# Kernel optimization log

Hardware: AMD Instinct MI355X
Metric: run time of the kernel (lower is better)

Reference implementation:

```python
import jax, jax.numpy as jnp
import numpy as np

N, IN, HID, OUT = 8192, 512, 256, 128

def setup_inputs() -> dict:
    key = jax.random.key(0)
    k1, k2, k3, k4 = jax.random.split(key, 4)
    adj = jax.random.uniform(k1, (N, N), dtype=jnp.float32)
    feature = jax.random.normal(k2, (N, IN), dtype=jnp.float32)
    W1 = jax.random.normal(k3, (IN, HID), dtype=jnp.float32) * (1.0 / np.sqrt(IN))
    b1 = jnp.zeros((HID,), dtype=jnp.float32)
    W2 = jax.random.normal(k4, (HID, OUT), dtype=jnp.float32) * (1.0 / np.sqrt(HID))
    b2 = jnp.zeros((OUT,), dtype=jnp.float32)
    return {"adj": adj, "feature": feature, "W1": W1, "b1": b1, "W2": W2, "b2": b2}

def reference(adj, feature, W1, b1, W2, b2):
    # GCN encoder: layer1 (relu) then layer2 (linear output)
    h = jax.nn.relu(adj @ (feature @ W1) + b1)   # [N, HID]
    h = adj @ (h @ W2) + b2                      # [N, OUT]
    # InnerProductDecoder: sigmoid(flatten(h @ h.T))
    logits = h @ h.T                             # [N, N]
    h_noise = jax.nn.sigmoid(logits.reshape(-1)) # [N*N]
    return (h_noise, h)
```

## Files before the change

kernel.cpp:

```cpp
#include <hip/hip_runtime.h>


typedef __bf16 bf16x8_t __attribute__((ext_vector_type(8)));
typedef __bf16 bf16x4_t __attribute__((ext_vector_type(4)));
typedef float  f32x4_t  __attribute__((ext_vector_type(4)));

#define MFMA_BF16(a, b, c) __builtin_amdgcn_mfma_f32_16x16x32_bf16((a), (b), (c), 0, 0, 0)

__device__ __forceinline__ bf16x8_t cvt8(f32x4_t u, f32x4_t v) {
    bf16x8_t o;
    o[0] = (__bf16)u[0]; o[1] = (__bf16)u[1]; o[2] = (__bf16)u[2]; o[3] = (__bf16)u[3];
    o[4] = (__bf16)v[0]; o[5] = (__bf16)v[1]; o[6] = (__bf16)v[2]; o[7] = (__bf16)v[3];
    return o;
}

__device__ __forceinline__ f32x4_t nt_load4(const float* p) {
    return __builtin_nontemporal_load((const f32x4_t*)p);
}
__device__ __forceinline__ void nt_store4(f32x4_t v, float* p) {
    __builtin_nontemporal_store(v, (f32x4_t*)p);
}

template<int AUX>
__device__ __forceinline__ void gload_lds16(const float* g, float* l) {
    __builtin_amdgcn_global_load_lds(
        (const __attribute__((address_space(1))) unsigned int*)g,
        (__attribute__((address_space(3))) unsigned int*)l, 16, 0, AUX);
}

__global__ __launch_bounds__(256) void cast_all(
    const float* __restrict__ feat, const float* __restrict__ W1,
    const float* __restrict__ W2, __bf16* __restrict__ fb,
    __bf16* __restrict__ w1t, __bf16* __restrict__ w2t)
{
    const int j = blockIdx.x * 256 + threadIdx.x;
    if (j < 524288) {
        const float* p = feat + (size_t)j * 8;
        f32x4_t u = nt_load4(p);
        f32x4_t v = nt_load4(p + 4);
        *(bf16x8_t*)(fb + (size_t)j * 8) = cvt8(u, v);
    } else if (j < 524288 + 131072) {
        int t = j - 524288;
        int k = t >> 8, n = t & 255;
        w1t[n * 512 + k] = (__bf16)W1[t];
    } else if (j < 524288 + 131072 + 32768) {
        int t = j - 655360;
        int k = t >> 7, n = t & 127;
        w2t[n * 256 + k] = (__bf16)W2[t];
    }
}

template<int MT, int WC>
__global__ __launch_bounds__(256, 2) void gemm_bt_cbf16(
    const __bf16* __restrict__ X, const __bf16* __restrict__ Yb,
    __bf16* __restrict__ C, int K, int N)
{
    constexpr int WR = 4 / WC;
    constexpr int BM = WR * MT * 16;
    constexpr int BN = WC * 64;
    const int mblk = blockIdx.x, nblk = blockIdx.y;
    const int w = threadIdx.x >> 6, lane = threadIdx.x & 63;
    const int wr = w / WC, wc = w % WC;
    const int q = lane >> 4, l16 = lane & 15;
    const int mbase = mblk * BM + wr * (MT * 16);
    const int nbase = nblk * BN + wc * 64;

    f32x4_t acc[MT][4];
    const f32x4_t z = {0.f, 0.f, 0.f, 0.f};
#pragma unroll
    for (int i = 0; i < MT; i++)
#pragma unroll
        for (int jj = 0; jj < 4; jj++) acc[i][jj] = z;

    const __bf16* Xr[MT];
    const __bf16* Yr[4];
#pragma unroll
    for (int i = 0; i < MT; i++) Xr[i] = X + (size_t)(mbase + i * 16 + l16) * K + q * 8;
#pragma unroll
    for (int jj = 0; jj < 4; jj++) Yr[jj] = Yb + (size_t)(nbase + jj * 16 + l16) * K + q * 8;

    for (int k = 0; k < K; k += 32) {
        bf16x8_t a[MT], b[4];
#pragma unroll
        for (int i = 0; i < MT; i++) a[i] = *(const bf16x8_t*)(Xr[i] + k);
#pragma unroll
        for (int jj = 0; jj < 4; jj++) b[jj] = *(const bf16x8_t*)(Yr[jj] + k);
#pragma unroll
        for (int i = 0; i < MT; i++)
#pragma unroll
            for (int jj = 0; jj < 4; jj++) acc[i][jj] = MFMA_BF16(a[i], b[jj], acc[i][jj]);
    }

#pragma unroll
    for (int i = 0; i < MT; i++)
#pragma unroll
        for (int jj = 0; jj < 4; jj++) {
            const int row0 = mbase + i * 16 + q * 4;
            const int col = nbase + jj * 16 + l16;
#pragma unroll
            for (int r = 0; r < 4; r++)
                C[(size_t)(row0 + r) * N + col] = (__bf16)acc[i][jj][r];
        }
}

template<int NN>
__global__ __launch_bounds__(256, 2) void gemm_adj_lds(
    const float* __restrict__ A, const __bf16* __restrict__ Y,
    float* __restrict__ P, int kchunk)
{
    constexpr int NT = NN / 64;
    __shared__ float As[2][4096];

    const int mblk = blockIdx.x;
    const int ks = blockIdx.y;
    const int w = threadIdx.x >> 6, lane = threadIdx.x & 63;
    const int q = lane >> 4, l16 = lane & 15;
    const int kbase = ks * kchunk;
    const int ntiles = kchunk >> 6;

    const int lrow = lane >> 4;
    const int lg = lane & 15;
    const float* gsrc[4];
    int loff[4];
#pragma unroll
    for (int j = 0; j < 4; j++) {
        const int row = j * 16 + w * 4 + lrow;
        const int colswz = ((lg ^ (row & 15)) << 2);
        gsrc[j] = A + (size_t)(mblk * 64 + row) * 8192 + kbase + colswz;
        loff[j] = row * 64 + (lg << 2);
    }

    const __bf16* Yr[NT];
#pragma unroll
    for (int jj = 0; jj < NT; jj++)
        Yr[jj] = Y + (size_t)(w * (NN / 4) + jj * 16 + l16) * 8192 + q * 8;

    f32x4_t acc[4][NT];
    const f32x4_t z = {0.f, 0.f, 0.f, 0.f};
#pragma unroll
    for (int i = 0; i < 4; i++)
#pragma unroll
        for (int jj = 0; jj < NT; jj++) acc[i][jj] = z;

#pragma unroll
    for (int j = 0; j < 4; j++) gload_lds16<2>(gsrc[j], &As[0][0] + loff[j]);

    int buf = 0;
    for (int kt = 0; kt < ntiles; kt++) {
        const int kk = kbase + (kt << 6);

        bf16x8_t breg[2][NT];
#pragma unroll
        for (int s = 0; s < 2; s++)
#pragma unroll
            for (int jj = 0; jj < NT; jj++)
                breg[s][jj] = *(const bf16x8_t*)(Yr[jj] + kk + s * 32);

        __syncthreads();

        if (kt + 1 < ntiles) {
            const int koff = (kt + 1) << 6;
#pragma unroll
            for (int j = 0; j < 4; j++)
                gload_lds16<2>(gsrc[j] + koff, &As[buf ^ 1][0] + loff[j]);
        }

        const float* __restrict__ L = &As[buf][0];
#pragma unroll
        for (int s = 0; s < 2; s++) {
            bf16x8_t a[4];
#pragma unroll
            for (int i = 0; i < 4; i++) {
                const int r = i * 16 + l16;
                const int g0 = ((s * 8 + q * 2) ^ l16) << 2;
                const int g1 = ((s * 8 + q * 2 + 1) ^ l16) << 2;
                f32x4_t u = *(const f32x4_t*)(L + r * 64 + g0);
                f32x4_t v = *(const f32x4_t*)(L + r * 64 + g1);
                a[i] = cvt8(u, v);
            }
#pragma unroll
            for (int i = 0; i < 4; i++)
#pragma unroll
                for (int jj = 0; jj < NT; jj++)
                    acc[i][jj] = MFMA_BF16(a[i], breg[s][jj], acc[i][jj]);
        }
        buf ^= 1;
    }

#pragma unroll
    for (int i = 0; i < 4; i++) {
        const int row0 = mblk * 64 + i * 16 + q * 4;
#pragma unroll
        for (int r = 0; r < 4; r++) {
            float* pp = P + ((size_t)ks * 8192 + row0 + r) * NN + w * (NN / 4) + l16;
#pragma unroll
            for (int jj = 0; jj < NT; jj++)
                __builtin_nontemporal_store(acc[i][jj][r], pp + jj * 16);
        }
    }
}

__global__ __launch_bounds__(256) void epi_relu_bias(
    const float* __restrict__ P, const float* __restrict__ bias,
    __bf16* __restrict__ H)
{
    const size_t SL = (size_t)8192 * 256;
    const size_t idx = ((size_t)blockIdx.x * 256 + threadIdx.x) * 4;
    f32x4_t s0 = nt_load4(P + idx);
    f32x4_t s1 = nt_load4(P + SL + idx);
    f32x4_t s2 = nt_load4(P + 2 * SL + idx);
    f32x4_t s3 = nt_load4(P + 3 * SL + idx);
    const int col = (int)(idx & 255);
    f32x4_t bb = *(const f32x4_t*)(bias + col);
    bf16x4_t o;
#pragma unroll
    for (int e = 0; e < 4; e++)
        o[e] = (__bf16)fmaxf(s0[e] + s1[e] + s2[e] + s3[e] + bb[e], 0.f);
    *(bf16x4_t*)(H + idx) = o;
}

__global__ __launch_bounds__(256) void epi_bias_out(
    const float* __restrict__ P, const float* __restrict__ bias,
    float* __restrict__ Hout, __bf16* __restrict__ Hbf)
{
    const size_t SL = (size_t)8192 * 128;
    const size_t idx = ((size_t)blockIdx.x * 256 + threadIdx.x) * 4;
    f32x4_t s0 = nt_load4(P + idx);
    f32x4_t s1 = nt_load4(P + SL + idx);
    f32x4_t s2 = nt_load4(P + 2 * SL + idx);
    f32x4_t s3 = nt_load4(P + 3 * SL + idx);
    const int col = (int)(idx & 127);
    f32x4_t bb = *(const f32x4_t*)(bias + col);
    f32x4_t o;
#pragma unroll
    for (int e = 0; e < 4; e++)
        o[e] = s0[e] + s1[e] + s2[e] + s3[e] + bb[e];
    nt_store4(o, Hout + idx);
    bf16x4_t ob;
#pragma unroll
    for (int e = 0; e < 4; e++) ob[e] = (__bf16)o[e];
    *(bf16x4_t*)(Hbf + idx) = ob;
}

__global__ __launch_bounds__(256, 4) void gemm_sig(
    const __bf16* __restrict__ H, float* __restrict__ out)
{
    __shared__ float S[64 * 132];

    const int mblk = blockIdx.x, nblk = blockIdx.y;
    const int w = threadIdx.x >> 6, lane = threadIdx.x & 63;
    const int wr = w >> 1, wc = w & 1;
    const int q = lane >> 4, l16 = lane & 15;
    const int mbase = mblk * 128 + wr * 64;
    const int nbase = nblk * 128 + wc * 64;

    f32x4_t acc[4][4];
    const f32x4_t z = {0.f, 0.f, 0.f, 0.f};
#pragma unroll
    for (int i = 0; i < 4; i++)
#pragma unroll
        for (int jj = 0; jj < 4; jj++) acc[i][jj] = z;

#pragma unroll
    for (int k = 0; k < 128; k += 32) {
        bf16x8_t a[4], b[4];
#pragma unroll
        for (int i = 0; i < 4; i++)
            a[i] = *(const bf16x8_t*)(H + (size_t)(mbase + i * 16 + l16) * 128 + k + q * 8);
#pragma unroll
        for (int jj = 0; jj < 4; jj++)
            b[jj] = *(const bf16x8_t*)(H + (size_t)(nbase + jj * 16 + l16) * 128 + k + q * 8);
#pragma unroll
        for (int i = 0; i < 4; i++)
#pragma unroll
            for (int jj = 0; jj < 4; jj++) acc[i][jj] = MFMA_BF16(a[i], b[jj], acc[i][jj]);
    }

#pragma unroll
    for (int h = 0; h < 2; h++) {
        if (h) __syncthreads();
#pragma unroll
        for (int i = 0; i < 2; i++) {
            const int ii = h * 2 + i;
            const int lrow = wr * 32 + i * 16 + q * 4;
#pragma unroll
            for (int jj = 0; jj < 4; jj++) {
                const int col = wc * 64 + jj * 16 + l16;
#pragma unroll
                for (int r = 0; r < 4; r++) {
                    const float x = acc[ii][jj][r];
                    S[(lrow + r) * 132 + col] = 1.0f / (1.0f + __expf(-x));
                }
            }
        }
        __syncthreads();
#pragma unroll
        for (int it = 0; it < 8; it++) {
            const int gid = it * 256 + (int)threadIdx.x;
            const int lr = gid >> 5;
            const int qd = gid & 31;
            f32x4_t v = *(const f32x4_t*)(S + lr * 132 + qd * 4);
            const int grow = mblk * 128 + (lr >> 5) * 64 + (lr & 31) + h * 32;
            const int gcol = nblk * 128 + qd * 4;
            nt_store4(v, out + (size_t)grow * 8192 + gcol);
        }
    }
}

extern "C" void kernel_launch(void* const* d_in, const int* in_sizes, int n_in,
                              void* d_out, int out_size, void* d_ws, size_t ws_size,
                              hipStream_t stream)
{
    const float* adj  = (const float*)d_in[0];
    const float* feat = (const float*)d_in[1];
    const float* W1   = (const float*)d_in[2];
    const float* b1   = (const float*)d_in[3];
    const float* W2   = (const float*)d_in[4];
    const float* b2   = (const float*)d_in[5];
    float* out = (float*)d_out;

    char* p = (char*)d_ws;
    __bf16* featbf = (__bf16*)p; p += (size_t)8192 * 512 * 2;
    __bf16* W1T    = (__bf16*)p; p += (size_t)256 * 512 * 2;
    __bf16* W2T    = (__bf16*)p; p += (size_t)128 * 256 * 2;
    __bf16* t1T    = (__bf16*)p; p += (size_t)256 * 8192 * 2;
    __bf16* h1     = (__bf16*)p; p += (size_t)8192 * 256 * 2;
    __bf16* t2T    = (__bf16*)p; p += (size_t)128 * 8192 * 2;
    __bf16* hbf    = (__bf16*)p; p += (size_t)8192 * 128 * 2;
    float* part    = (float*)p;

    cast_all<<<2688, 256, 0, stream>>>(feat, W1, W2, featbf, W1T, W2T);
    gemm_bt_cbf16<2, 2><<<dim3(4, 64), 256, 0, stream>>>(W1T, featbf, t1T, 512, 8192);
    gemm_adj_lds<256><<<dim3(128, 4), 256, 0, stream>>>(adj, t1T, part, 2048);
    epi_relu_bias<<<2048, 256, 0, stream>>>(part, b1, h1);
    gemm_bt_cbf16<2, 2><<<dim3(2, 64), 256, 0, stream>>>(W2T, h1, t2T, 256, 8192);
    gemm_adj_lds<128><<<dim3(128, 4), 256, 0, stream>>>(adj, t2T, part, 2048);
    epi_bias_out<<<1024, 256, 0, stream>>>(part, b2, out + (size_t)8192 * 8192, hbf);
    gemm_sig<<<dim3(64, 64), 256, 0, stream>>>(hbf, out);
}
```

Measured before the change: 639.3 us.

## Load adjacency tiles directly into registers instead of staging through LDS

The adjacency GEMM kernel stops double-buffering A tiles in shared memory with global_load_lds and __syncthreads. Each wave now reads its A fragments from global memory straight into registers with nontemporal loads, software-pipelined in two 32-wide k halves, and converts them to bf16 there. This removes the LDS traffic, the swizzle arithmetic and the block barriers. In exchange, all four waves in a block load the same A rows, so cache-level traffic roughly quadruples. With nontemporal hints those redundant reads may miss cache and reach HBM.

```diff
diff --git a/kernel.cpp b/kernel.cpp
--- a/kernel.cpp
+++ b/kernel.cpp
@@ -19,13 +19,6 @@
 }
 __device__ __forceinline__ void nt_store4(f32x4_t v, float* p) {
     __builtin_nontemporal_store(v, (f32x4_t*)p);
-}
-
-template<int AUX>
-__device__ __forceinline__ void gload_lds16(const float* g, float* l) {
-    __builtin_amdgcn_global_load_lds(
-        (const __attribute__((address_space(1))) unsigned int*)g,
-        (__attribute__((address_space(3))) unsigned int*)l, 16, 0, AUX);
 }
 
 __global__ __launch_bounds__(256) void cast_all(
@@ -104,36 +97,26 @@
 }
 
 template<int NN>
-__global__ __launch_bounds__(256, 2) void gemm_adj_lds(
+__global__ __launch_bounds__(256, 2) void gemm_adj_direct(
     const float* __restrict__ A, const __bf16* __restrict__ Y,
     float* __restrict__ P, int kchunk)
 {
     constexpr int NT = NN / 64;
-    __shared__ float As[2][4096];
-
     const int mblk = blockIdx.x;
     const int ks = blockIdx.y;
     const int w = threadIdx.x >> 6, lane = threadIdx.x & 63;
     const int q = lane >> 4, l16 = lane & 15;
     const int kbase = ks * kchunk;
-    const int ntiles = kchunk >> 6;
-
-    const int lrow = lane >> 4;
-    const int lg = lane & 15;
-    const float* gsrc[4];
-    int loff[4];
-#pragma unroll
-    for (int j = 0; j < 4; j++) {
-        const int row = j * 16 + w * 4 + lrow;
-        const int colswz = ((lg ^ (row & 15)) << 2);
-        gsrc[j] = A + (size_t)(mblk * 64 + row) * 8192 + kbase + colswz;
-        loff[j] = row * 64 + (lg << 2);
-    }
+
+    const float* Ar[4];
+#pragma unroll
+    for (int i = 0; i < 4; i++)
+        Ar[i] = A + (size_t)(mblk * 64 + i * 16 + l16) * 8192 + kbase + q * 8;
 
     const __bf16* Yr[NT];
 #pragma unroll
     for (int jj = 0; jj < NT; jj++)
-        Yr[jj] = Y + (size_t)(w * (NN / 4) + jj * 16 + l16) * 8192 + q * 8;
+        Yr[jj] = Y + (size_t)(w * (NN / 4) + jj * 16 + l16) * 8192 + kbase + q * 8;
 
     f32x4_t acc[4][NT];
     const f32x4_t z = {0.f, 0.f, 0.f, 0.f};
@@ -142,49 +125,59 @@
 #pragma unroll
         for (int jj = 0; jj < NT; jj++) acc[i][jj] = z;
 
-#pragma unroll
-    for (int j = 0; j < 4; j++) gload_lds16<2>(gsrc[j], &As[0][0] + loff[j]);
-
-    int buf = 0;
-    for (int kt = 0; kt < ntiles; kt++) {
-        const int kk = kbase + (kt << 6);
-
-        bf16x8_t breg[2][NT];
-#pragma unroll
-        for (int s = 0; s < 2; s++)
+    f32x4_t ua[4], va[4], ub[4], vb[4];
+    bf16x8_t bfa[NT], bfb[NT];
+
+#pragma unroll
+    for (int i = 0; i < 4; i++) {
+        ua[i] = nt_load4(Ar[i]);
+        va[i] = nt_load4(Ar[i] + 4);
+    }
+#pragma unroll
+    for (int jj = 0; jj < NT; jj++) bfa[jj] = *(const bf16x8_t*)(Yr[jj]);
+
+    for (int k = 0; k < kchunk; k += 64) {
+#pragma unroll
+        for (int i = 0; i < 4; i++) {
+            ub[i] = nt_load4(Ar[i] + k + 32);
+            vb[i] = nt_load4(Ar[i] + k + 36);
+        }
+#pragma unroll
+        for (int jj = 0; jj < NT; jj++)
+            bfb[jj] = *(const bf16x8_t*)(Yr[jj] + k + 32);
+
+        {
+            bf16x8_t afr[4];
+#pragma unroll
+            for (int i = 0; i < 4; i++) afr[i] = cvt8(ua[i], va[i]);
+#pragma unroll
+            for (int i = 0; i < 4; i++)
+#pragma unroll
+                for (int jj = 0; jj < NT; jj++)
+                    acc[i][jj] = MFMA_BF16(afr[i], bfa[jj], acc[i][jj]);
+        }
+
+        if (k + 64 < kchunk) {
+#pragma unroll
+            for (int i = 0; i < 4; i++) {
+                ua[i] = nt_load4(Ar[i] + k + 64);
+                va[i] = nt_load4(Ar[i] + k + 68);
+            }
 #pragma unroll
             for (int jj = 0; jj < NT; jj++)
-                breg[s][jj] = *(const bf16x8_t*)(Yr[jj] + kk + s * 32);
-
-        __syncthreads();
-
-        if (kt + 1 < ntiles) {
-            const int koff = (kt + 1) << 6;
-#pragma unroll
-            for (int j = 0; j < 4; j++)
-                gload_lds16<2>(gsrc[j] + koff, &As[buf ^ 1][0] + loff[j]);
-        }
-
-        const float* __restrict__ L = &As[buf][0];
-#pragma unroll
-        for (int s = 0; s < 2; s++) {
-            bf16x8_t a[4];
-#pragma unroll
-            for (int i = 0; i < 4; i++) {
-                const int r = i * 16 + l16;
-                const int g0 = ((s * 8 + q * 2) ^ l16) << 2;
-                const int g1 = ((s * 8 + q * 2 + 1) ^ l16) << 2;
-                f32x4_t u = *(const f32x4_t*)(L + r * 64 + g0);
-                f32x4_t v = *(const f32x4_t*)(L + r * 64 + g1);
-                a[i] = cvt8(u, v);
-            }
+                bfa[jj] = *(const bf16x8_t*)(Yr[jj] + k + 64);
+        }
+
+        {
+            bf16x8_t afr[4];
+#pragma unroll
+            for (int i = 0; i < 4; i++) afr[i] = cvt8(ub[i], vb[i]);
 #pragma unroll
             for (int i = 0; i < 4; i++)
 #pragma unroll
                 for (int jj = 0; jj < NT; jj++)
-                    acc[i][jj] = MFMA_BF16(a[i], breg[s][jj], acc[i][jj]);
-        }
-        buf ^= 1;
+                    acc[i][jj] = MFMA_BF16(afr[i], bfb[jj], acc[i][jj]);
+        }
     }
 
 #pragma unroll
@@ -331,10 +324,10 @@
 
     cast_all<<<2688, 256, 0, stream>>>(feat, W1, W2, featbf, W1T, W2T);
     gemm_bt_cbf16<2, 2><<<dim3(4, 64), 256, 0, stream>>>(W1T, featbf, t1T, 512, 8192);
-    gemm_adj_lds<256><<<dim3(128, 4), 256, 0, stream>>>(adj, t1T, part, 2048);
+    gemm_adj_direct<256><<<dim3(128, 4), 256, 0, stream>>>(adj, t1T, part, 2048);
     epi_relu_bias<<<2048, 256, 0, stream>>>(part, b1, h1);
     gemm_bt_cbf16<2, 2><<<dim3(2, 64), 256, 0, stream>>>(W2T, h1, t2T, 256, 8192);
-    gemm_adj_lds<128><<<dim3(128, 4), 256, 0, stream>>>(adj, t2T, part, 2048);
+    gemm_adj_direct<128><<<dim3(128, 4), 256, 0, stream>>>(adj, t2T, part, 2048);
     epi_bias_out<<<1024, 256, 0, stream>>>(part, b2, out + (size_t)8192 * 8192, hbf);
     gemm_sig<<<dim3(64, 64), 256, 0, stream>>>(hbf, out);
 }
```

New measurement: 1.011 ms. 1.58x slower.
